# Optimization experiments

Measured on AMD Instinct MI355X. Metric: run time of the kernel, lower is better.

Reference implementation:

```python
import jax, jax.numpy as jnp
import numpy as np

N_NODES = 250000
N_EDGES = 5000000


def setup_inputs() -> dict:
    key = jax.random.key(0)
    k1, k2, k3, k4, k5, k6 = jax.random.split(key, 6)
    x = jax.random.normal(k1, (N_NODES, 1), dtype=jnp.float32)
    edge_index = jax.random.randint(k2, (2, N_EDGES), 0, N_NODES, dtype=jnp.int64)
    # Glorot-style small weights like PyG GCNConv init
    W1 = jax.random.normal(k3, (1, 16), dtype=jnp.float32) * (1.0 / np.sqrt(1 + 16))
    b1 = jnp.zeros((16,), dtype=jnp.float32)
    W2 = jax.random.normal(k4, (16, 2), dtype=jnp.float32) * (1.0 / np.sqrt(16 + 2))
    b2 = jnp.zeros((2,), dtype=jnp.float32)
    return {"x": x, "edge_index": edge_index, "W1": W1, "b1": b1, "W2": W2, "b2": b2}


def _gcn_conv(x, row, col, W, b, n_nodes):
    """PyG GCNConv: x' = D^{-1/2} (A + I) D^{-1/2} (x W) + b.

    row = source nodes, col = target nodes (messages flow row -> col).
    Self-loops are assumed already appended to row/col.
    """
    h = x @ W  # [N, out]
    ones = jnp.ones(row.shape[0], dtype=h.dtype)
    deg = jax.ops.segment_sum(ones, col, num_segments=n_nodes)  # in-degree incl. self-loop
    dinv = jnp.where(deg > 0, jax.lax.rsqrt(deg), 0.0)
    norm = dinv[row] * dinv[col]  # [E+N]
    msg = h[row] * norm[:, None]  # gather + scale  [E+N, out]
    out = jax.ops.segment_sum(msg, col, num_segments=n_nodes)  # scatter-add
    return out + b


def reference(x, edge_index, W1, b1, W2, b2):
    n = x.shape[0]
    loop = jnp.arange(n, dtype=edge_index.dtype)
    row = jnp.concatenate([edge_index[0], loop])
    col = jnp.concatenate([edge_index[1], loop])
    h = _gcn_conv(x, row, col, W1, b1, n)
    h = jax.nn.relu(h)
    # F.dropout(training=False) at inference -> identity
    h = _gcn_conv(h, row, col, W2, b2, n)
    return jax.nn.softmax(h, axis=1)
```

## Files before the change

### kernel.cpp

```cpp
#include <hip/hip_runtime.h>

#define ST 512
#define PT 20
#define EPB (ST * PT)
#define CSHIFT 9
#define CMASK 511u
#define CW 512
#define CAP 12288


__device__ __forceinline__ void sort_body(const int* __restrict__ row,
                                          const int* __restrict__ col,
                                          unsigned* __restrict__ gcur,
                                          unsigned* __restrict__ pack1,
                                          int E, int NC, int b, int t) {
    __shared__ unsigned cnt[CW];
    __shared__ unsigned cur[CW];
    cnt[t] = 0;
    __syncthreads();
    int base = b * EPB;
    int c[PT];
#pragma unroll
    for (int k = 0; k < PT / 4; ++k) {
        int e = base + (k * ST + t) * 4;
        int4 cc;
        if (e + 3 < E) {
            cc = *reinterpret_cast<const int4*>(col + e);
        } else {
            cc.x = (e     < E) ? col[e]     : -1;
            cc.y = (e + 1 < E) ? col[e + 1] : -1;
            cc.z = (e + 2 < E) ? col[e + 2] : -1;
            cc.w = (e + 3 < E) ? col[e + 3] : -1;
        }
        c[4 * k] = cc.x; c[4 * k + 1] = cc.y; c[4 * k + 2] = cc.z; c[4 * k + 3] = cc.w;
    }
#pragma unroll
    for (int k = 0; k < PT; ++k)
        if (c[k] >= 0) atomicAdd(&cnt[(unsigned)c[k] >> CSHIFT], 1u);
    __syncthreads();
    if (t < NC) cur[t] = atomicAdd(&gcur[t], cnt[t]);
    __syncthreads();
#pragma unroll
    for (int k = 0; k < PT / 4; ++k) {
        int e = base + (k * ST + t) * 4;
        int4 rr = make_int4(0, 0, 0, 0);
        if (e + 3 < E) {
            rr = *reinterpret_cast<const int4*>(row + e);
        } else {
            rr.x = (e     < E) ? row[e]     : 0;
            rr.y = (e + 1 < E) ? row[e + 1] : 0;
            rr.z = (e + 2 < E) ? row[e + 2] : 0;
            rr.w = (e + 3 < E) ? row[e + 3] : 0;
        }
        int rl[4] = {rr.x, rr.y, rr.z, rr.w};
#pragma unroll
        for (int j = 0; j < 4; ++j) {
            int cc = c[4 * k + j];
            if (cc >= 0) {
                unsigned bb = (unsigned)cc >> CSHIFT;
                unsigned pos = atomicAdd(&cur[bb], 1u);
                if (pos < (bb + 1u) * CAP)
                    pack1[pos] = ((unsigned)rl[j] << CSHIFT) | ((unsigned)cc & CMASK);
            }
        }
    }
}

__device__ __forceinline__ void deg_body(const unsigned* __restrict__ pack1,
                                         const float* __restrict__ x,
                                         float* __restrict__ dinv, float* __restrict__ xs,
                                         unsigned s0, unsigned s1, int N, int b, int t) {
    __shared__ unsigned dcnt[CW];
    dcnt[t] = 0;
    __syncthreads();
    unsigned n4 = (s1 - s0) >> 2;
    for (unsigned i = t; i < n4; i += ST) {
        uint4 p = reinterpret_cast<const uint4*>(pack1 + s0)[i];
        atomicAdd(&dcnt[p.x & CMASK], 1u);
        atomicAdd(&dcnt[p.y & CMASK], 1u);
        atomicAdd(&dcnt[p.z & CMASK], 1u);
        atomicAdd(&dcnt[p.w & CMASK], 1u);
    }
    unsigned i = s0 + (n4 << 2) + t;
    if (i < s1) atomicAdd(&dcnt[pack1[i] & CMASK], 1u);
    __syncthreads();
    int v = (b << CSHIFT) + t;
    if (v < N) {
        float di = rsqrtf((float)dcnt[t] + 1.0f);
        dinv[v] = di;
        xs[v] = di * x[v];
    }
}

__device__ __forceinline__ void l1_body(const unsigned* __restrict__ pack1,
                                        const float* __restrict__ xs,
                                        const float* __restrict__ dinv,
                                        const float* __restrict__ W1,
                                        const float* __restrict__ b1,
                                        const float* __restrict__ W2,
                                        float* __restrict__ gs,
                                        unsigned s0, unsigned s1, int N, int b, int t) {
    __shared__ float acc[CW];
    acc[t] = 0.0f;
    __syncthreads();
    unsigned n4 = (s1 - s0) >> 2;
    for (unsigned i = t; i < n4; i += ST) {
        uint4 p = reinterpret_cast<const uint4*>(pack1 + s0)[i];
        float v0 = xs[p.x >> CSHIFT];
        float v1 = xs[p.y >> CSHIFT];
        float v2 = xs[p.z >> CSHIFT];
        float v3 = xs[p.w >> CSHIFT];
        atomicAdd(&acc[p.x & CMASK], v0);
        atomicAdd(&acc[p.y & CMASK], v1);
        atomicAdd(&acc[p.z & CMASK], v2);
        atomicAdd(&acc[p.w & CMASK], v3);
    }
    unsigned i = s0 + (n4 << 2) + t;
    if (i < s1) {
        unsigned p = pack1[i];
        atomicAdd(&acc[p & CMASK], xs[p >> CSHIFT]);
    }
    __syncthreads();
    int v = (b << CSHIFT) + t;
    if (v < N) {
        float di = dinv[v];
        float tt = di * (acc[t] + xs[v]);
        float g = 0.0f;
#pragma unroll
        for (int j = 0; j < 16; ++j) {
            float y = fmaxf(fmaf(W1[j], tt, b1[j]), 0.0f);
            g = fmaf(W2[2 * j] - W2[2 * j + 1], y, g);
        }
        gs[v] = di * g;
    }
}

__device__ __forceinline__ void l2_body(const unsigned* __restrict__ pack1,
                                        const float* __restrict__ gs,
                                        const float* __restrict__ dinv,
                                        const float* __restrict__ b2,
                                        float* __restrict__ out,
                                        unsigned s0, unsigned s1, int N, int b, int t) {
    __shared__ float acc[CW];
    acc[t] = 0.0f;
    __syncthreads();
    unsigned n4 = (s1 - s0) >> 2;
    for (unsigned i = t; i < n4; i += ST) {
        uint4 p = reinterpret_cast<const uint4*>(pack1 + s0)[i];
        float v0 = gs[p.x >> CSHIFT];
        float v1 = gs[p.y >> CSHIFT];
        float v2 = gs[p.z >> CSHIFT];
        float v3 = gs[p.w >> CSHIFT];
        atomicAdd(&acc[p.x & CMASK], v0);
        atomicAdd(&acc[p.y & CMASK], v1);
        atomicAdd(&acc[p.z & CMASK], v2);
        atomicAdd(&acc[p.w & CMASK], v3);
    }
    unsigned i = s0 + (n4 << 2) + t;
    if (i < s1) {
        unsigned p = pack1[i];
        atomicAdd(&acc[p & CMASK], gs[p >> CSHIFT]);
    }
    __syncthreads();
    int v = (b << CSHIFT) + t;
    if (v < N) {
        float diff = dinv[v] * (acc[t] + gs[v]) + (b2[0] - b2[1]);
        float p0 = 1.0f / (1.0f + __expf(-diff));
        float2 o;
        o.x = p0;
        o.y = 1.0f - p0;
        reinterpret_cast<float2*>(out)[v] = o;
    }
}

__global__ void k_init(unsigned* __restrict__ gcur, int NC) {
    for (int b = threadIdx.x + blockIdx.x * blockDim.x; b < NC; b += blockDim.x * gridDim.x)
        gcur[b] = (unsigned)b * CAP;
}
__global__ __launch_bounds__(ST) void k_sortk(const int* __restrict__ row,
                                              const int* __restrict__ col,
                                              unsigned* __restrict__ gcur,
                                              unsigned* __restrict__ pack1, int E, int NC) {
    sort_body(row, col, gcur, pack1, E, NC, blockIdx.x, threadIdx.x);
}
__global__ __launch_bounds__(ST) void k_degk(const unsigned* __restrict__ pack1,
                                             const unsigned* __restrict__ gcur,
                                             const float* __restrict__ x,
                                             float* __restrict__ dinv, float* __restrict__ xs,
                                             int N) {
    int b = blockIdx.x;
    unsigned s0 = (unsigned)b * CAP;
    unsigned s1 = min(gcur[b], s0 + (unsigned)CAP);
    deg_body(pack1, x, dinv, xs, s0, s1, N, b, threadIdx.x);
}
__global__ __launch_bounds__(ST) void k_l1k(const unsigned* __restrict__ pack1,
                                            const unsigned* __restrict__ gcur,
                                            const float* __restrict__ xs,
                                            const float* __restrict__ dinv,
                                            const float* __restrict__ W1,
                                            const float* __restrict__ b1,
                                            const float* __restrict__ W2,
                                            float* __restrict__ gs, int N) {
    int b = blockIdx.x;
    unsigned s0 = (unsigned)b * CAP;
    unsigned s1 = min(gcur[b], s0 + (unsigned)CAP);
    l1_body(pack1, xs, dinv, W1, b1, W2, gs, s0, s1, N, b, threadIdx.x);
}
__global__ __launch_bounds__(ST) void k_l2k(const unsigned* __restrict__ pack1,
                                            const unsigned* __restrict__ gcur,
                                            const float* __restrict__ gs,
                                            const float* __restrict__ dinv,
                                            const float* __restrict__ b2,
                                            float* __restrict__ out, int N) {
    int b = blockIdx.x;
    unsigned s0 = (unsigned)b * CAP;
    unsigned s1 = min(gcur[b], s0 + (unsigned)CAP);
    l2_body(pack1, gs, dinv, b2, out, s0, s1, N, b, threadIdx.x);
}

__global__ void k_zero_f(float* __restrict__ p, int n) {
    int i = blockIdx.x * blockDim.x + threadIdx.x;
    int v = i * 4;
    if (v + 3 < n) {
        reinterpret_cast<float4*>(p + v)[0] = make_float4(0.f, 0.f, 0.f, 0.f);
    } else {
        for (; v < n; ++v) p[v] = 0.0f;
    }
}
__global__ void k_deg_f(const int* __restrict__ col, float* __restrict__ deg, int E) {
    int i = blockIdx.x * blockDim.x + threadIdx.x;
    int e = i * 4;
    if (e + 3 < E) {
        int4 c = reinterpret_cast<const int4*>(col + e)[0];
        atomicAdd(deg + c.x, 1.0f); atomicAdd(deg + c.y, 1.0f);
        atomicAdd(deg + c.z, 1.0f); atomicAdd(deg + c.w, 1.0f);
    } else {
        for (; e < E; ++e) atomicAdd(deg + col[e], 1.0f);
    }
}
__global__ void k_node1_f(const float* __restrict__ x, float* __restrict__ degdinv,
                          float* __restrict__ xs, int N) {
    int v = blockIdx.x * blockDim.x + threadIdx.x;
    if (v < N) {
        float dinv = rsqrtf(degdinv[v] + 1.0f);
        degdinv[v] = dinv;
        xs[v] = dinv * x[v];
    }
}
__global__ void k_scat_f(const int* __restrict__ row, const int* __restrict__ col,
                         const float* __restrict__ src, float* __restrict__ acc, int E) {
    int i = blockIdx.x * blockDim.x + threadIdx.x;
    int e = i * 4;
    if (e + 3 < E) {
        int4 r = reinterpret_cast<const int4*>(row + e)[0];
        int4 c = reinterpret_cast<const int4*>(col + e)[0];
        float s0 = src[r.x], s1 = src[r.y], s2 = src[r.z], s3 = src[r.w];
        atomicAdd(acc + c.x, s0); atomicAdd(acc + c.y, s1);
        atomicAdd(acc + c.z, s2); atomicAdd(acc + c.w, s3);
    } else {
        for (; e < E; ++e) atomicAdd(acc + col[e], src[row[e]]);
    }
}
__global__ void k_mlp_f(const float* __restrict__ W1, const float* __restrict__ b1,
                        const float* __restrict__ W2, const float* __restrict__ dinv,
                        float* __restrict__ acc, float* __restrict__ xsgs, int N) {
    int v = blockIdx.x * blockDim.x + threadIdx.x;
    if (v < N) {
        float di = dinv[v];
        float t = di * (acc[v] + xsgs[v]);
        float g = 0.0f;
#pragma unroll
        for (int j = 0; j < 16; ++j) {
            float y = fmaxf(fmaf(W1[j], t, b1[j]), 0.0f);
            g = fmaf(W2[2 * j] - W2[2 * j + 1], y, g);
        }
        xsgs[v] = di * g;
        acc[v] = 0.0f;
    }
}
__global__ void k_out_f(const float* __restrict__ b2, const float* __restrict__ dinv,
                        const float* __restrict__ acc, const float* __restrict__ gs,
                        float* __restrict__ out, int N) {
    int v = blockIdx.x * blockDim.x + threadIdx.x;
    if (v < N) {
        float diff = dinv[v] * (acc[v] + gs[v]) + (b2[0] - b2[1]);
        float p0 = 1.0f / (1.0f + __expf(-diff));
        float2 o; o.x = p0; o.y = 1.0f - p0;
        reinterpret_cast<float2*>(out)[v] = o;
    }
}

extern "C" void kernel_launch(void* const* d_in, const int* in_sizes, int n_in,
                              void* d_out, int out_size, void* d_ws, size_t ws_size,
                              hipStream_t stream) {
    const float* x  = (const float*)d_in[0];
    const int* edge = (const int*)d_in[1];
    const float* W1 = (const float*)d_in[2];
    const float* b1 = (const float*)d_in[3];
    const float* W2 = (const float*)d_in[4];
    const float* b2 = (const float*)d_in[5];
    float* out = (float*)d_out;

    const int N = in_sizes[0];
    const int E = in_sizes[1] / 2;
    const int* row = edge;
    const int* col = edge + E;

    const int NC  = (N + CW - 1) >> CSHIFT;
    const int NBS = (E + EPB - 1) / EPB;

    const double mean = (double)E / NC;
    const double slack = mean + 8.0 * __builtin_sqrt(mean > 1.0 ? mean : 1.0);
    const size_t need = ((size_t)NC * CAP + NC) * 4 + (size_t)3 * N * 4;

    if (NC <= CW && N < (1 << 23) && slack < CAP && ws_size >= need) {
        unsigned* pack1 = (unsigned*)d_ws;
        unsigned* gcur  = pack1 + (size_t)NC * CAP;
        float* dinv     = (float*)(gcur + NC);
        float* xs       = dinv + N;
        float* gs       = xs + N;

        k_init <<<1, 512, 0, stream>>>(gcur, NC);
        k_sortk<<<NBS, ST, 0, stream>>>(row, col, gcur, pack1, E, NC);
        k_degk <<<NC, ST, 0, stream>>>(pack1, gcur, x, dinv, xs, N);
        k_l1k  <<<NC, ST, 0, stream>>>(pack1, gcur, xs, dinv, W1, b1, W2, gs, N);
        k_l2k  <<<NC, ST, 0, stream>>>(pack1, gcur, gs, dinv, b2, out, N);
    } else {
        float* w0 = (float*)d_ws;
        float* w1 = w0 + N;
        float* w2 = w1 + N;
        const int nb = (N + 255) / 256;
        const int eb = ((E + 3) / 4 + 255) / 256;
        const int zb = ((2 * N + 3) / 4 + 255) / 256;
        k_zero_f <<<zb, 256, 0, stream>>>(w0, 2 * N);
        k_deg_f  <<<eb, 256, 0, stream>>>(col, w0, E);
        k_node1_f<<<nb, 256, 0, stream>>>(x, w0, w2, N);
        k_scat_f <<<eb, 256, 0, stream>>>(row, col, w2, w1, E);
        k_mlp_f  <<<nb, 256, 0, stream>>>(W1, b1, W2, w0, w1, w2, N);
        k_scat_f <<<eb, 256, 0, stream>>>(row, col, w2, w1, E);
        k_out_f  <<<nb, 256, 0, stream>>>(b2, w0, w1, w2, out, N);
    }
}
```

Baseline: 194.4 us.

## Stage bucketed edges in LDS for coalesced writes and widen buckets to 1024 nodes

The sort kernel now builds local bucket offsets with a shared-memory prefix scan and writes packed edges into a 40KB LDS staging buffer. It then copies them out to global memory contiguously, finding each element's bucket by binary search. Before, each edge went straight to a scattered global address. Buckets are widened from 512 to 1024 nodes, which halves the bucket count and doubles each bucket's capacity, so the deg, l1 and l2 kernels each handle two nodes per thread. This targets uncoalesced global scatter writes, at the cost of more LDS per block (lower occupancy), scan barriers, and a binary search per element.

```diff
diff --git a/kernel.cpp b/kernel.cpp
--- a/kernel.cpp
+++ b/kernel.cpp
@@ -3,23 +3,35 @@
 #define ST 512
 #define PT 20
 #define EPB (ST * PT)
-#define CSHIFT 9
-#define CMASK 511u
-#define CW 512
-#define CAP 12288
-
-
-__device__ __forceinline__ void sort_body(const int* __restrict__ row,
-                                          const int* __restrict__ col,
-                                          unsigned* __restrict__ gcur,
-                                          unsigned* __restrict__ pack1,
-                                          int E, int NC, int b, int t) {
-    __shared__ unsigned cnt[CW];
-    __shared__ unsigned cur[CW];
-    cnt[t] = 0;
-    __syncthreads();
-    int base = b * EPB;
+#define CSHIFT 10
+#define CMASK 1023u
+#define CW 1024
+#define NCMAX 256
+#define CAP 24576
+
+
+__global__ void k_init(unsigned* __restrict__ gcur, int NC) {
+    for (int b = threadIdx.x; b < NC; b += blockDim.x)
+        gcur[b] = (unsigned)b * CAP;
+}
+
+__global__ __launch_bounds__(ST) void k_sortk(const int* __restrict__ row,
+                                              const int* __restrict__ col,
+                                              unsigned* __restrict__ gcur,
+                                              unsigned* __restrict__ pack1,
+                                              int E, int NC) {
+    __shared__ unsigned loff[NCMAX + 1];
+    __shared__ unsigned gbase[NCMAX];
+    __shared__ unsigned cur[NCMAX];
+    __shared__ unsigned staging[EPB];
+
+    const int t = threadIdx.x;
+    for (int i = t; i <= NC; i += ST) loff[i] = 0;
+    __syncthreads();
+
+    const int base = blockIdx.x * EPB;
     int c[PT];
+
 #pragma unroll
     for (int k = 0; k < PT / 4; ++k) {
         int e = base + (k * ST + t) * 4;
@@ -36,10 +48,24 @@
     }
 #pragma unroll
     for (int k = 0; k < PT; ++k)
-        if (c[k] >= 0) atomicAdd(&cnt[(unsigned)c[k] >> CSHIFT], 1u);
-    __syncthreads();
-    if (t < NC) cur[t] = atomicAdd(&gcur[t], cnt[t]);
-    __syncthreads();
+        if (c[k] >= 0) atomicAdd(&loff[((unsigned)c[k] >> CSHIFT) + 1], 1u);
+    __syncthreads();
+
+    for (int o = 1; o <= NC; o <<= 1) {
+        unsigned v = 0;
+        if (t <= NC && t >= o) v = loff[t - o];
+        __syncthreads();
+        if (t <= NC) loff[t] += v;
+        __syncthreads();
+    }
+
+    if (t < NC) {
+        unsigned cb = loff[t + 1] - loff[t];
+        gbase[t] = atomicAdd(&gcur[t], cb);
+        cur[t] = loff[t];
+    }
+    __syncthreads();
+
 #pragma unroll
     for (int k = 0; k < PT / 4; ++k) {
         int e = base + (k * ST + t) * 4;
@@ -57,22 +83,40 @@
         for (int j = 0; j < 4; ++j) {
             int cc = c[4 * k + j];
             if (cc >= 0) {
-                unsigned bb = (unsigned)cc >> CSHIFT;
-                unsigned pos = atomicAdd(&cur[bb], 1u);
-                if (pos < (bb + 1u) * CAP)
-                    pack1[pos] = ((unsigned)rl[j] << CSHIFT) | ((unsigned)cc & CMASK);
+                unsigned b = (unsigned)cc >> CSHIFT;
+                unsigned p = atomicAdd(&cur[b], 1u);
+                staging[p] = ((unsigned)rl[j] << CSHIFT) | ((unsigned)cc & CMASK);
             }
         }
     }
-}
-
-__device__ __forceinline__ void deg_body(const unsigned* __restrict__ pack1,
-                                         const float* __restrict__ x,
-                                         float* __restrict__ dinv, float* __restrict__ xs,
-                                         unsigned s0, unsigned s1, int N, int b, int t) {
+    __syncthreads();
+
+    const unsigned tot = loff[NC];
+    for (unsigned i = t; i < tot; i += ST) {
+        unsigned lo = 0, hi = (unsigned)NC;
+        while (hi - lo > 1) {
+            unsigned mid = (lo + hi) >> 1;
+            if (loff[mid] <= i) lo = mid; else hi = mid;
+        }
+        unsigned pos = gbase[lo] + (i - loff[lo]);
+        if (pos < (lo + 1u) * CAP)
+            pack1[pos] = staging[i];
+    }
+}
+
+
+__global__ __launch_bounds__(ST) void k_degk(const unsigned* __restrict__ pack1,
+                                             const unsigned* __restrict__ gcur,
+                                             const float* __restrict__ x,
+                                             float* __restrict__ dinv, float* __restrict__ xs,
+                                             int N) {
     __shared__ unsigned dcnt[CW];
-    dcnt[t] = 0;
-    __syncthreads();
+    const int b = blockIdx.x;
+    const int t = threadIdx.x;
+    dcnt[t] = 0; dcnt[t + ST] = 0;
+    __syncthreads();
+    unsigned s0 = (unsigned)b * CAP;
+    unsigned s1 = min(gcur[b], s0 + (unsigned)CAP);
     unsigned n4 = (s1 - s0) >> 2;
     for (unsigned i = t; i < n4; i += ST) {
         uint4 p = reinterpret_cast<const uint4*>(pack1 + s0)[i];
@@ -84,25 +128,33 @@
     unsigned i = s0 + (n4 << 2) + t;
     if (i < s1) atomicAdd(&dcnt[pack1[i] & CMASK], 1u);
     __syncthreads();
-    int v = (b << CSHIFT) + t;
-    if (v < N) {
-        float di = rsqrtf((float)dcnt[t] + 1.0f);
-        dinv[v] = di;
-        xs[v] = di * x[v];
-    }
-}
-
-__device__ __forceinline__ void l1_body(const unsigned* __restrict__ pack1,
-                                        const float* __restrict__ xs,
-                                        const float* __restrict__ dinv,
-                                        const float* __restrict__ W1,
-                                        const float* __restrict__ b1,
-                                        const float* __restrict__ W2,
-                                        float* __restrict__ gs,
-                                        unsigned s0, unsigned s1, int N, int b, int t) {
+#pragma unroll
+    for (int j = 0; j < 2; ++j) {
+        int tl = t + j * ST;
+        int v = (b << CSHIFT) + tl;
+        if (v < N) {
+            float di = rsqrtf((float)dcnt[tl] + 1.0f);
+            dinv[v] = di;
+            xs[v] = di * x[v];
+        }
+    }
+}
+
+__global__ __launch_bounds__(ST) void k_l1k(const unsigned* __restrict__ pack1,
+                                            const unsigned* __restrict__ gcur,
+                                            const float* __restrict__ xs,
+                                            const float* __restrict__ dinv,
+                                            const float* __restrict__ W1,
+                                            const float* __restrict__ b1,
+                                            const float* __restrict__ W2,
+                                            float* __restrict__ gs, int N) {
     __shared__ float acc[CW];
-    acc[t] = 0.0f;
-    __syncthreads();
+    const int b = blockIdx.x;
+    const int t = threadIdx.x;
+    acc[t] = 0.0f; acc[t + ST] = 0.0f;
+    __syncthreads();
+    unsigned s0 = (unsigned)b * CAP;
+    unsigned s1 = min(gcur[b], s0 + (unsigned)CAP);
     unsigned n4 = (s1 - s0) >> 2;
     for (unsigned i = t; i < n4; i += ST) {
         uint4 p = reinterpret_cast<const uint4*>(pack1 + s0)[i];
@@ -121,29 +173,37 @@
         atomicAdd(&acc[p & CMASK], xs[p >> CSHIFT]);
     }
     __syncthreads();
-    int v = (b << CSHIFT) + t;
-    if (v < N) {
-        float di = dinv[v];
-        float tt = di * (acc[t] + xs[v]);
-        float g = 0.0f;
-#pragma unroll
-        for (int j = 0; j < 16; ++j) {
-            float y = fmaxf(fmaf(W1[j], tt, b1[j]), 0.0f);
-            g = fmaf(W2[2 * j] - W2[2 * j + 1], y, g);
-        }
-        gs[v] = di * g;
-    }
-}
-
-__device__ __forceinline__ void l2_body(const unsigned* __restrict__ pack1,
-                                        const float* __restrict__ gs,
-                                        const float* __restrict__ dinv,
-                                        const float* __restrict__ b2,
-                                        float* __restrict__ out,
-                                        unsigned s0, unsigned s1, int N, int b, int t) {
+#pragma unroll
+    for (int j = 0; j < 2; ++j) {
+        int tl = t + j * ST;
+        int v = (b << CSHIFT) + tl;
+        if (v < N) {
+            float di = dinv[v];
+            float tt = di * (acc[tl] + xs[v]);
+            float g = 0.0f;
+#pragma unroll
+            for (int jj = 0; jj < 16; ++jj) {
+                float y = fmaxf(fmaf(W1[jj], tt, b1[jj]), 0.0f);
+                g = fmaf(W2[2 * jj] - W2[2 * jj + 1], y, g);
+            }
+            gs[v] = di * g;
+        }
+    }
+}
+
+__global__ __launch_bounds__(ST) void k_l2k(const unsigned* __restrict__ pack1,
+                                            const unsigned* __restrict__ gcur,
+                                            const float* __restrict__ gs,
+                                            const float* __restrict__ dinv,
+                                            const float* __restrict__ b2,
+                                            float* __restrict__ out, int N) {
     __shared__ float acc[CW];
-    acc[t] = 0.0f;
-    __syncthreads();
+    const int b = blockIdx.x;
+    const int t = threadIdx.x;
+    acc[t] = 0.0f; acc[t + ST] = 0.0f;
+    __syncthreads();
+    unsigned s0 = (unsigned)b * CAP;
+    unsigned s1 = min(gcur[b], s0 + (unsigned)CAP);
     unsigned n4 = (s1 - s0) >> 2;
     for (unsigned i = t; i < n4; i += ST) {
         uint4 p = reinterpret_cast<const uint4*>(pack1 + s0)[i];
@@ -162,60 +222,19 @@
         atomicAdd(&acc[p & CMASK], gs[p >> CSHIFT]);
     }
     __syncthreads();
-    int v = (b << CSHIFT) + t;
-    if (v < N) {
-        float diff = dinv[v] * (acc[t] + gs[v]) + (b2[0] - b2[1]);
-        float p0 = 1.0f / (1.0f + __expf(-diff));
-        float2 o;
-        o.x = p0;
-        o.y = 1.0f - p0;
-        reinterpret_cast<float2*>(out)[v] = o;
-    }
-}
-
-__global__ void k_init(unsigned* __restrict__ gcur, int NC) {
-    for (int b = threadIdx.x + blockIdx.x * blockDim.x; b < NC; b += blockDim.x * gridDim.x)
-        gcur[b] = (unsigned)b * CAP;
-}
-__global__ __launch_bounds__(ST) void k_sortk(const int* __restrict__ row,
-                                              const int* __restrict__ col,
-                                              unsigned* __restrict__ gcur,
-                                              unsigned* __restrict__ pack1, int E, int NC) {
-    sort_body(row, col, gcur, pack1, E, NC, blockIdx.x, threadIdx.x);
-}
-__global__ __launch_bounds__(ST) void k_degk(const unsigned* __restrict__ pack1,
-                                             const unsigned* __restrict__ gcur,
-                                             const float* __restrict__ x,
-                                             float* __restrict__ dinv, float* __restrict__ xs,
-                                             int N) {
-    int b = blockIdx.x;
-    unsigned s0 = (unsigned)b * CAP;
-    unsigned s1 = min(gcur[b], s0 + (unsigned)CAP);
-    deg_body(pack1, x, dinv, xs, s0, s1, N, b, threadIdx.x);
-}
-__global__ __launch_bounds__(ST) void k_l1k(const unsigned* __restrict__ pack1,
-                                            const unsigned* __restrict__ gcur,
-                                            const float* __restrict__ xs,
-                                            const float* __restrict__ dinv,
-                                            const float* __restrict__ W1,
-                                            const float* __restrict__ b1,
-                                            const float* __restrict__ W2,
-                                            float* __restrict__ gs, int N) {
-    int b = blockIdx.x;
-    unsigned s0 = (unsigned)b * CAP;
-    unsigned s1 = min(gcur[b], s0 + (unsigned)CAP);
-    l1_body(pack1, xs, dinv, W1, b1, W2, gs, s0, s1, N, b, threadIdx.x);
-}
-__global__ __launch_bounds__(ST) void k_l2k(const unsigned* __restrict__ pack1,
-                                            const unsigned* __restrict__ gcur,
-                                            const float* __restrict__ gs,
-                                            const float* __restrict__ dinv,
-                                            const float* __restrict__ b2,
-                                            float* __restrict__ out, int N) {
-    int b = blockIdx.x;
-    unsigned s0 = (unsigned)b * CAP;
-    unsigned s1 = min(gcur[b], s0 + (unsigned)CAP);
-    l2_body(pack1, gs, dinv, b2, out, s0, s1, N, b, threadIdx.x);
+#pragma unroll
+    for (int j = 0; j < 2; ++j) {
+        int tl = t + j * ST;
+        int v = (b << CSHIFT) + tl;
+        if (v < N) {
+            float diff = dinv[v] * (acc[tl] + gs[v]) + (b2[0] - b2[1]);
+            float p0 = 1.0f / (1.0f + __expf(-diff));
+            float2 o;
+            o.x = p0;
+            o.y = 1.0f - p0;
+            reinterpret_cast<float2*>(out)[v] = o;
+        }
+    }
 }
 
 __global__ void k_zero_f(float* __restrict__ p, int n) {
@@ -313,14 +332,14 @@
     const double slack = mean + 8.0 * __builtin_sqrt(mean > 1.0 ? mean : 1.0);
     const size_t need = ((size_t)NC * CAP + NC) * 4 + (size_t)3 * N * 4;
 
-    if (NC <= CW && N < (1 << 23) && slack < CAP && ws_size >= need) {
+    if (NC <= NCMAX && N < (1 << 22) && slack < CAP && ws_size >= need) {
         unsigned* pack1 = (unsigned*)d_ws;
         unsigned* gcur  = pack1 + (size_t)NC * CAP;
         float* dinv     = (float*)(gcur + NC);
         float* xs       = dinv + N;
         float* gs       = xs + N;
 
-        k_init <<<1, 512, 0, stream>>>(gcur, NC);
+        k_init <<<1, 256, 0, stream>>>(gcur, NC);
         k_sortk<<<NBS, ST, 0, stream>>>(row, col, gcur, pack1, E, NC);
         k_degk <<<NC, ST, 0, stream>>>(pack1, gcur, x, dinv, xs, N);
         k_l1k  <<<NC, ST, 0, stream>>>(pack1, gcur, xs, dinv, W1, b1, W2, gs, N);
```

New measurement: 183.1 us. -5.8%, faster.
